# Optimization experiments

Hardware: AMD Instinct MI355X
Metric: run time of the kernel (lower is better)

## Reference

```python
import jax, jax.numpy as jnp
import numpy as np

B, N = 4, 512           # batch of graphs, nodes per graph
D = 3 * N               # H is a (3N, 3N) block matrix of 3x3 rotations


def _build_indices():
    # Upper-triangular edge list (i < j), M = N(N-1)/2 edges
    i, j = np.triu_indices(N, k=1)
    M = i.shape[0]
    b = np.arange(B)[:, None, None, None]
    r = np.arange(3)[None, None, :, None]
    c = np.arange(3)[None, None, None, :]

    def pack(rows, cols):
        bb = np.broadcast_to(b, (B, M, 3, 3))
        rw = np.broadcast_to(rows, (B, M, 3, 3))
        cl = np.broadcast_to(cols, (B, M, 3, 3))
        return np.stack([bb, rw, cl], axis=-1).reshape(-1, 3).astype(np.int32)

    # (b, 3i+r, 3j+c): the (i,j) 3x3 block of H
    gi = pack(3 * i[None, :, None, None] + r, 3 * j[None, :, None, None] + c)
    # (b, 3j+r, 3i+c): the (j,i) 3x3 block of H
    gi2 = pack(3 * j[None, :, None, None] + r, 3 * i[None, :, None, None] + c)
    # (b, j): sign source node per edge for the J-ambiguity indicator
    bu = np.broadcast_to(np.arange(B)[:, None], (B, M))
    ju = np.broadcast_to(j[None, :], (B, M))
    u_idx = np.stack([bu, ju], axis=-1).reshape(-1, 2).astype(np.int32)
    return jnp.asarray(gi), jnp.asarray(gi2), jnp.asarray(u_idx)


def setup_inputs() -> dict:
    key = jax.random.key(0)
    k1, k2 = jax.random.split(key)
    H = jax.random.normal(k1, (B, D, D), dtype=jnp.float32)
    u_s = jax.random.normal(k2, (B, N), dtype=jnp.float32)
    gi, gi2, u_idx = _build_indices()
    return {"H": H, "u_s": u_s, "gather_idx": gi, "gather_idx2": gi2,
            "u_s_gather_idx": u_idx}


def reference(H, u_s, gather_idx, gather_idx2, u_s_gather_idx):
    Bn = H.shape[0]
    # indicator: 1.0 where gathered u_s entry < 0, shape (B, M)
    ind = (u_s[u_s_gather_idx[:, 0], u_s_gather_idx[:, 1]] < 0)
    ind = ind.reshape(Bn, -1).astype(H.dtype)
    # gather the (i,j) and (j,i) 3x3 blocks -> (B, M, 3, 3)
    Hg = H[gather_idx[:, 0], gather_idx[:, 1], gather_idx[:, 2]].reshape(Bn, -1, 3, 3)
    Hg2 = H[gather_idx2[:, 0], gather_idx2[:, 1], gather_idx2[:, 2]].reshape(Bn, -1, 3, 3)
    # J_mat = indicator * diag(1,1,-1) + (1 - indicator) * I3
    I3 = jnp.eye(3, dtype=H.dtype)
    Jd = jnp.diag(jnp.asarray([1.0, 1.0, -1.0], dtype=H.dtype))
    indb = ind[..., None, None]
    J = indb * Jd + (1.0 - indb) * I3          # (B, M, 3, 3)
    Hc = J @ Hg @ J
    Hc2 = J @ Hg2 @ J
    # scatter_nd adds for duplicate indices; the two scatters are summed
    out = jnp.zeros_like(H)
    out = out.at[gather_idx[:, 0], gather_idx[:, 1], gather_idx[:, 2]].add(Hc.reshape(-1))
    out = out.at[gather_idx2[:, 0], gather_idx2[:, 1], gather_idx2[:, 2]].add(Hc2.reshape(-1))
    return out
```

## Files before the change

kernel.cpp:

```cpp
#include <hip/hip_runtime.h>

__global__ void jflip_kernel(const float* __restrict__ H,
                             const float* __restrict__ u_s,
                             float* __restrict__ out,
                             int N, int D) {
    const int b = blockIdx.y;
    const int R = blockIdx.x;
    const int p = R / 3;
    const int r = R - 3 * p;
    const bool r2 = (r == 2);

    const long long rowOff = (long long)b * D * D + (long long)R * D;
    const int C0 = threadIdx.x * 4;
    if (C0 >= D) return;

    const float* usb = u_s + (long long)b * N;

    float4 h = *reinterpret_cast<const float4*>(H + rowOff + C0);
    float hv[4] = {h.x, h.y, h.z, h.w};
    float ov[4];

#pragma unroll
    for (int k = 0; k < 4; ++k) {
        const int C = C0 + k;
        const int q = C / 3;
        const int c = C - 3 * q;
        if (q == p) {
            ov[k] = 0.0f;
        } else {
            const int mx = (p > q) ? p : q;
            const bool ind = usb[mx] < 0.0f;
            const bool flip = ind && (r2 != (c == 2));
            ov[k] = flip ? -hv[k] : hv[k];
        }
    }

    float4 o = make_float4(ov[0], ov[1], ov[2], ov[3]);
    *reinterpret_cast<float4*>(out + rowOff + C0) = o;
}

extern "C" void kernel_launch(void* const* d_in, const int* in_sizes, int n_in,
                              void* d_out, int out_size, void* d_ws, size_t ws_size,
                              hipStream_t stream) {
    const float* H   = (const float*)d_in[0];
    const float* u_s = (const float*)d_in[1];
    float* out = (float*)d_out;

    const long long nH  = (long long)in_sizes[0];
    const long long nUs = (long long)in_sizes[1];
    const int N = (int)(nH / (9LL * nUs));
    const int B = (int)(nUs / N);
    const int D = 3 * N;

    dim3 grid((unsigned)D, (unsigned)B);
    dim3 block((unsigned)(D / 4));

    jflip_kernel<<<grid, block, 0, stream>>>(H, u_s, out, N, D);
}
```

Baseline: 19.28 us.

## Process four node-columns per thread and four rows per block

Each thread now handles 12 contiguous columns (four 3x3 block columns) with three float4 loads, and each block covers four rows, shrinking the grid fourfold. The per-element division by 3 and scattered u_s lookups are replaced by one float4 load of u_s plus a single u_s[p] value, with the min/max choice done by comparison. Hardcoded 128 threads in x assumes D=1536 (N=512), and the early bounds check is removed.

```diff
diff --git a/kernel.cpp b/kernel.cpp
--- a/kernel.cpp
+++ b/kernel.cpp
@@ -1,42 +1,52 @@
 #include <hip/hip_runtime.h>
 
-__global__ void jflip_kernel(const float* __restrict__ H,
-                             const float* __restrict__ u_s,
-                             float* __restrict__ out,
-                             int N, int D) {
+__global__ __launch_bounds__(512)
+void jflip_kernel(const float* __restrict__ H,
+                  const float* __restrict__ u_s,
+                  float* __restrict__ out,
+                  int N, int D) {
     const int b = blockIdx.y;
-    const int R = blockIdx.x;
+    const int R = blockIdx.x * 4 + threadIdx.y;
     const int p = R / 3;
     const int r = R - 3 * p;
     const bool r2 = (r == 2);
 
-    const long long rowOff = (long long)b * D * D + (long long)R * D;
-    const int C0 = threadIdx.x * 4;
-    if (C0 >= D) return;
+    const int t    = threadIdx.x;
+    const int q0   = t * 4;
+    const int col0 = t * 12;
 
     const float* usb = u_s + (long long)b * N;
+    const long long off = ((long long)b * D + R) * D + col0;
 
-    float4 h = *reinterpret_cast<const float4*>(H + rowOff + C0);
-    float hv[4] = {h.x, h.y, h.z, h.w};
-    float ov[4];
+    const float4 h0 = *reinterpret_cast<const float4*>(H + off);
+    const float4 h1 = *reinterpret_cast<const float4*>(H + off + 4);
+    const float4 h2 = *reinterpret_cast<const float4*>(H + off + 8);
+    const float4 u4 = *reinterpret_cast<const float4*>(usb + q0);
+    const float  up = usb[p];
+
+    const float hv[12] = {h0.x, h0.y, h0.z, h0.w,
+                          h1.x, h1.y, h1.z, h1.w,
+                          h2.x, h2.y, h2.z, h2.w};
+    const float uv[4]  = {u4.x, u4.y, u4.z, u4.w};
+    float ov[12];
 
 #pragma unroll
-    for (int k = 0; k < 4; ++k) {
-        const int C = C0 + k;
-        const int q = C / 3;
-        const int c = C - 3 * q;
-        if (q == p) {
-            ov[k] = 0.0f;
-        } else {
-            const int mx = (p > q) ? p : q;
-            const bool ind = usb[mx] < 0.0f;
+    for (int j = 0; j < 4; ++j) {
+        const int q = q0 + j;
+        const bool diag = (q == p);
+        const bool ind  = ((q > p) ? uv[j] : up) < 0.0f;
+#pragma unroll
+        for (int c = 0; c < 3; ++c) {
+            const int m = 3 * j + c;
             const bool flip = ind && (r2 != (c == 2));
-            ov[k] = flip ? -hv[k] : hv[k];
+            const float v = flip ? -hv[m] : hv[m];
+            ov[m] = diag ? 0.0f : v;
         }
     }
 
-    float4 o = make_float4(ov[0], ov[1], ov[2], ov[3]);
-    *reinterpret_cast<float4*>(out + rowOff + C0) = o;
+    *reinterpret_cast<float4*>(out + off)     = make_float4(ov[0], ov[1], ov[2],  ov[3]);
+    *reinterpret_cast<float4*>(out + off + 4) = make_float4(ov[4], ov[5], ov[6],  ov[7]);
+    *reinterpret_cast<float4*>(out + off + 8) = make_float4(ov[8], ov[9], ov[10], ov[11]);
 }
 
 extern "C" void kernel_launch(void* const* d_in, const int* in_sizes, int n_in,
@@ -52,8 +62,8 @@
     const int B = (int)(nUs / N);
     const int D = 3 * N;
 
-    dim3 grid((unsigned)D, (unsigned)B);
-    dim3 block((unsigned)(D / 4));
+    dim3 block(128, 4);
+    dim3 grid((unsigned)(D / 4), (unsigned)B);
 
     jflip_kernel<<<grid, block, 0, stream>>>(H, u_s, out, N, D);
 }
```

Measured after the change: 20.04 us. 1.04x slower.

## Flatten elementwise J-flip into grid-stride loop with compile-time dims

Applied to the files above, without the earlier changes.

Replaces the per-row 2D grid (one block of D/4 threads per row) with a flat grid-stride loop over float4 elements using 256-thread blocks and a fixed 2048-block grid. A templated specialization makes D and N compile-time constants so index divisions become cheap multiplies. The sign logic is reformulated as float multipliers, with the row-node sign hoisted out of the inner loop. The aim is better occupancy and less index overhead, at the cost of 64-bit index math per iteration and a fixed grid size that may not match the CU count well.

```diff
diff --git a/kernel.cpp b/kernel.cpp
--- a/kernel.cpp
+++ b/kernel.cpp
@@ -1,42 +1,80 @@
 #include <hip/hip_runtime.h>
 
-__global__ void jflip_kernel(const float* __restrict__ H,
-                             const float* __restrict__ u_s,
-                             float* __restrict__ out,
-                             int N, int D) {
-    const int b = blockIdx.y;
-    const int R = blockIdx.x;
-    const int p = R / 3;
-    const int r = R - 3 * p;
-    const bool r2 = (r == 2);
 
-    const long long rowOff = (long long)b * D * D + (long long)R * D;
-    const int C0 = threadIdx.x * 4;
-    if (C0 >= D) return;
+typedef float v4f __attribute__((ext_vector_type(4)));
 
-    const float* usb = u_s + (long long)b * N;
+template <int D, int N>
+__global__ __launch_bounds__(256)
+void jflip_flat(const float* __restrict__ H,
+                const float* __restrict__ u_s,
+                float* __restrict__ out,
+                long long nV4) {
+    const long long stride = (long long)gridDim.x * blockDim.x;
+    long long f = (long long)blockIdx.x * blockDim.x + threadIdx.x;
 
-    float4 h = *reinterpret_cast<const float4*>(H + rowOff + C0);
-    float hv[4] = {h.x, h.y, h.z, h.w};
-    float ov[4];
+    constexpr int DD = D * D;
 
+    for (; f < nV4; f += stride) {
+        const long long idx = f * 4;
+        const int b   = (int)(idx / DD);
+        const int rem = (int)(idx - (long long)b * DD);
+        const int R   = rem / D;
+        const int C0  = rem - R * D;
+
+        const int p = R / 3;
+        const float r2s = ((R - 3 * p) == 2) ? -1.0f : 1.0f;
+        const float* usb = u_s + (long long)b * N;
+        const float sp = (usb[p] < 0.0f) ? -1.0f : 1.0f;
+
+        const v4f h = *reinterpret_cast<const v4f*>(H + idx);
+        v4f o;
 #pragma unroll
-    for (int k = 0; k < 4; ++k) {
-        const int C = C0 + k;
-        const int q = C / 3;
-        const int c = C - 3 * q;
-        if (q == p) {
-            ov[k] = 0.0f;
-        } else {
-            const int mx = (p > q) ? p : q;
-            const bool ind = usb[mx] < 0.0f;
-            const bool flip = ind && (r2 != (c == 2));
-            ov[k] = flip ? -hv[k] : hv[k];
+        for (int k = 0; k < 4; ++k) {
+            const int C = C0 + k;
+            const int q = C / 3;
+            const float c2s = ((C - 3 * q) == 2) ? -1.0f : 1.0f;
+            const float s   = (q > p) ? ((usb[q] < 0.0f) ? -1.0f : 1.0f) : sp;
+            const float mult = (s < 0.0f) ? (r2s * c2s) : 1.0f;
+            o[k] = (q == p) ? 0.0f : h[k] * mult;
         }
+        *reinterpret_cast<v4f*>(out + idx) = o;
     }
+}
 
-    float4 o = make_float4(ov[0], ov[1], ov[2], ov[3]);
-    *reinterpret_cast<float4*>(out + rowOff + C0) = o;
+__global__ __launch_bounds__(256)
+void jflip_flat_gen(const float* __restrict__ H,
+                    const float* __restrict__ u_s,
+                    float* __restrict__ out,
+                    int N, int D, long long nV4) {
+    const long long stride = (long long)gridDim.x * blockDim.x;
+    long long f = (long long)blockIdx.x * blockDim.x + threadIdx.x;
+    const int DD = D * D;
+
+    for (; f < nV4; f += stride) {
+        const long long idx = f * 4;
+        const int b   = (int)(idx / DD);
+        const int rem = (int)(idx - (long long)b * DD);
+        const int R   = rem / D;
+        const int C0  = rem - R * D;
+
+        const int p = R / 3;
+        const float r2s = ((R - 3 * p) == 2) ? -1.0f : 1.0f;
+        const float* usb = u_s + (long long)b * N;
+        const float sp = (usb[p] < 0.0f) ? -1.0f : 1.0f;
+
+        const v4f h = *reinterpret_cast<const v4f*>(H + idx);
+        v4f o;
+#pragma unroll
+        for (int k = 0; k < 4; ++k) {
+            const int C = C0 + k;
+            const int q = C / 3;
+            const float c2s = ((C - 3 * q) == 2) ? -1.0f : 1.0f;
+            const float s   = (q > p) ? ((usb[q] < 0.0f) ? -1.0f : 1.0f) : sp;
+            const float mult = (s < 0.0f) ? (r2s * c2s) : 1.0f;
+            o[k] = (q == p) ? 0.0f : h[k] * mult;
+        }
+        *reinterpret_cast<v4f*>(out + idx) = o;
+    }
 }
 
 extern "C" void kernel_launch(void* const* d_in, const int* in_sizes, int n_in,
@@ -52,8 +90,13 @@
     const int B = (int)(nUs / N);
     const int D = 3 * N;
 
-    dim3 grid((unsigned)D, (unsigned)B);
-    dim3 block((unsigned)(D / 4));
+    const long long nV4 = nH / 4;
+    dim3 block(256);
+    dim3 grid(2048);
 
-    jflip_kernel<<<grid, block, 0, stream>>>(H, u_s, out, N, D);
+    if (N == 512 && D == 1536) {
+        jflip_flat<1536, 512><<<grid, block, 0, stream>>>(H, u_s, out, nV4);
+    } else {
+        jflip_flat_gen<<<grid, block, 0, stream>>>(H, u_s, out, N, D, nV4);
+    }
 }
```

Result: faster. 17.35 us (-10.0%).
